# Optimization experiments

Hardware: AMD Instinct MI355X
Metric: run time of the kernel (lower is better)

## Reference

```python
import jax, jax.numpy as jnp
import numpy as np
from jax import lax


def _dtw_normalized(x, y):
    """DTW with symmetric2 step pattern and cityblock (L1) local cost on scalars.

    D[0,0] = d[0,0]; D[i,0] = D[i-1,0] + d[i,0]; D[0,j] = D[0,j-1] + d[0,j]
    D[i,j] = min(D[i-1,j-1] + 2*d, D[i-1,j] + d, D[i,j-1] + d)
    normalizedDistance = D[n-1,m-1] / (n + m)
    """
    n = x.shape[0]

    def row_update(d_prev, xi):
        d = jnp.abs(xi - y)              # local cost row, [m]
        first = d_prev[0] + d[0]         # D[i,0]

        def step(left, inp):
            dj, up, diag = inp
            val = jnp.minimum(jnp.minimum(diag + 2.0 * dj, up + dj), left + dj)
            return val, val

        _, rest = lax.scan(step, first, (d[1:], d_prev[1:], d_prev[:-1]))
        new_row = jnp.concatenate([first[None], rest])
        return new_row, None

    d0 = jnp.cumsum(jnp.abs(x[0] - y))   # D[0, :]
    d_last, _ = lax.scan(row_update, d0, x[1:])
    return d_last[-1] / (2.0 * n)        # n + m with n == m


def setup_inputs() -> dict:
    key = jax.random.key(0)
    k1, k2 = jax.random.split(key)
    x = jax.random.normal(k1, (64, 1024), dtype=jnp.float32)
    x_target = jax.random.normal(k2, (64, 1024), dtype=jnp.float32)
    return {"x": x, "x_target": x_target}


def reference(x, x_target):
    dists = jax.vmap(_dtw_normalized)(x, x_target)  # [bs]
    return jnp.mean(dists)
```

## Files before the change

kernel.cpp:

```cpp
#include <hip/hip_runtime.h>

#define SEQ_N 1024
#define BATCH 64
#define NW    4
#define RPL   4
#define KSL   32
#define DELTA 96
#define LAG   33
#define RINGN 160
#define PAD_F 352
#define PAD_B 384

__device__ __forceinline__ float wave_shr1(float v, float fill) {
    return __int_as_float(__builtin_amdgcn_update_dpp(
        __float_as_int(fill), __float_as_int(v), 0x138, 0xF, 0xF, false));
}

__global__ __launch_bounds__(256, 1) void dtw_kernel(const float* __restrict__ x,
                                                     const float* __restrict__ y,
                                                     float* __restrict__ dists) {
    __shared__ float sy_raw[PAD_F + SEQ_N + PAD_B];
    __shared__ float ring[NW - 1][RINGN];

    const int b   = blockIdx.x;
    const int tid = threadIdx.x;
    const int w   = tid >> 6;
    const int l   = tid & 63;
    const float INF = 3.0e37f;
    const int  off = w * DELTA + l;
    const bool is_ring_l0 = (l == 0) && (w > 0);
    const bool is_tid0 = (tid == 0);

    for (int i = tid; i < PAD_F; i += 256) sy_raw[i] = 0.0f;
    for (int i = tid; i < PAD_B; i += 256) sy_raw[PAD_F + SEQ_N + i] = 0.0f;
    ((float4*)(sy_raw + PAD_F))[tid] = ((const float4*)(y + b * SEQ_N))[tid];
    const float4 xv = *((const float4*)(x + b * SEQ_N + w * 256 + l * RPL));
    const float xr0 = xv.x, xr1 = xv.y, xr2 = xv.z, xr3 = xv.w;
    __syncthreads();

    const float* const yp = sy_raw + PAD_F - off;

    float c0 = INF, c1 = INF, c2 = INF, c3 = INF;
    float diag_top = INF, bottom = INF;
    float yA[KSL], yB[KSL], rb[KSL], bt[KSL];

    #pragma unroll
    for (int k = 0; k < KSL; ++k) yA[k] = yp[k];

#define EPOCH(MASKED, FIRST, S0, YU, YF)                                     \
  {                                                                          \
    __syncthreads();                                                         \
    if (w > 0) {                                                             \
      int rbase = ((S0) & 127) + 95; if (rbase >= 128) rbase -= 128;         \
      const float* rp = ring[w - 1] + rbase;                                 \
      _Pragma("unroll")                                                      \
      for (int k2 = 0; k2 < KSL; ++k2) rb[k2] = rp[k2];                      \
    } else {                                                                 \
      _Pragma("unroll")                                                      \
      for (int k2 = 0; k2 < KSL; ++k2) rb[k2] = INF;                         \
    }                                                                        \
    _Pragma("unroll")                                                        \
    for (int k2 = 0; k2 < KSL; ++k2) YF[k2] = yp[(S0) + KSL + k2];           \
    _Pragma("unroll")                                                        \
    for (int k2 = 0; k2 < KSL; ++k2) {                                       \
      const float up_dpp = wave_shr1(bottom, INF);                           \
      float upv = is_ring_l0 ? rb[k2] : up_dpp;                              \
      if ((FIRST) && k2 == 0 && is_tid0) upv = 0.0f;      \
      const float yj = YU[k2];                                               \
      bool act = true;                                                       \
      if (MASKED) act = ((unsigned)((S0) + k2 - off) < (unsigned)SEQ_N);     \
      if (act) {                                                             \
        const float d0 = xr0 - yj, d1 = xr1 - yj,                            \
                    d2 = xr2 - yj, d3 = xr3 - yj;                            \
        const float t0 = diag_top + fabsf(d0);                               \
        const float t1 = c0 + fabsf(d1);                                     \
        const float t2 = c1 + fabsf(d2);                                     \
        const float t3 = c2 + fabsf(d3);                                     \
        float v = upv;                                                       \
        v = fminf(fminf(t0, c0), v) + fabsf(d0); c0 = v;                     \
        v = fminf(fminf(t1, c1), v) + fabsf(d1); c1 = v;                     \
        v = fminf(fminf(t2, c2), v) + fabsf(d2); c2 = v;                     \
        v = fminf(fminf(t3, c3), v) + fabsf(d3); c3 = v;                     \
        diag_top = upv; bottom = v;                                          \
      }                                                                      \
      if ((FIRST) && k2 == 0 && is_tid0) diag_top = INF; \
      bt[k2] = bottom;                                                       \
    }                                                                        \
    if (w < NW - 1 && l == 63) {                                             \
      const int mm = (S0) & 127;                                             \
      float* wp = ring[w] + mm;                                              \
      _Pragma("unroll")                                                      \
      for (int k2 = 0; k2 < KSL; ++k2) wp[k2] = bt[k2];                      \
      if (mm == 0) {                                                         \
        _Pragma("unroll")                                                    \
        for (int k2 = 0; k2 < KSL; ++k2) ring[w][128 + k2] = bt[k2];         \
      }                                                                      \
    }                                                                        \
  }

    EPOCH(true, true, 0, yA, yB);
    int s0 = 32;
    for (int it = 0; it < 5; ++it) {
        EPOCH(true, false, s0, yB, yA);
        EPOCH(true, false, s0 + 32, yA, yB);
        s0 += 64;
    }
    for (int it = 0; it < 10; ++it) {
        EPOCH(false, false, s0, yB, yA);
        EPOCH(false, false, s0 + 32, yA, yB);
        s0 += 64;
    }
    for (int it = 0; it < 6; ++it) {
        EPOCH(true, false, s0, yB, yA);
        EPOCH(true, false, s0 + 32, yA, yB);
        s0 += 64;
    }
#undef EPOCH

    if (tid == 255) dists[b] = c3 * (1.0f / (2.0f * (float)SEQ_N));
}

__global__ void dtw_reduce_kernel(const float* __restrict__ dists,
                                  float* __restrict__ out) {
    float v = dists[threadIdx.x] * (1.0f / (float)BATCH);
    #pragma unroll
    for (int o = 32; o > 0; o >>= 1) v += __shfl_down(v, o);
    if (threadIdx.x == 0) out[0] = v;
}

extern "C" void kernel_launch(void* const* d_in, const int* in_sizes, int n_in,
                              void* d_out, int out_size, void* d_ws, size_t ws_size,
                              hipStream_t stream) {
    const float* x = (const float*)d_in[0];
    const float* y = (const float*)d_in[1];
    float* out = (float*)d_out;
    float* dists = (float*)d_ws;

    dtw_kernel<<<BATCH, 256, 0, stream>>>(x, y, dists);
    dtw_reduce_kernel<<<1, BATCH, 0, stream>>>(dists, out);
}
```

Baseline: 89.02 us.

## Split DTW into bidirectional half-sweeps meeting at middle column and stitch

Each batch's DTW is split into a forward sweep over the first 512 columns and a backward sweep over the reversed last 512 columns, run as separate blocks (128 blocks instead of 64). A new stitch kernel combines the two half-cost columns at the midpoint by taking a minimum over rows. This halves the serial wavefront length per block and uses more CUs. In exchange the backward sweep carries extra local-cost state, there is an extra kernel launch and workspace traffic, and the stitch logic at the boundary must be exact for correctness.

```diff
diff --git a/kernel.cpp b/kernel.cpp
--- a/kernel.cpp
+++ b/kernel.cpp
@@ -3,56 +3,74 @@
 #define SEQ_N 1024
 #define BATCH 64
 #define NW    4
-#define RPL   4
 #define KSL   32
 #define DELTA 96
-#define LAG   33
 #define RINGN 160
 #define PAD_F 352
 #define PAD_B 384
+#define NPAIR 512
+#define SYN   (PAD_F + NPAIR + PAD_B)
 
 __device__ __forceinline__ float wave_shr1(float v, float fill) {
     return __int_as_float(__builtin_amdgcn_update_dpp(
         __float_as_int(fill), __float_as_int(v), 0x138, 0xF, 0xF, false));
 }
 
-__global__ __launch_bounds__(256, 1) void dtw_kernel(const float* __restrict__ x,
-                                                     const float* __restrict__ y,
-                                                     float* __restrict__ dists) {
-    __shared__ float sy_raw[PAD_F + SEQ_N + PAD_B];
-    __shared__ float ring[NW - 1][RINGN];
-
-    const int b   = blockIdx.x;
+__global__ __launch_bounds__(256, 1) void dtw_sweep_kernel(const float* __restrict__ x,
+                                                           const float* __restrict__ y,
+                                                           float* __restrict__ wsF,
+                                                           float* __restrict__ wsP) {
+    __shared__ float  sy_raw[SYN];
+    __shared__ float  ringF[NW - 1][RINGN];
+    __shared__ float2 ringB[NW - 1][RINGN];
+
+    const int bid = blockIdx.x;
+    const int dir = bid >> 6;
+    const int b   = bid & 63;
     const int tid = threadIdx.x;
     const int w   = tid >> 6;
     const int l   = tid & 63;
     const float INF = 3.0e37f;
     const int  off = w * DELTA + l;
     const bool is_ring_l0 = (l == 0) && (w > 0);
-    const bool is_tid0 = (tid == 0);
+    const bool is_seed = (tid == 0);
+    const int  r0 = w * 256 + l * 4;
 
     for (int i = tid; i < PAD_F; i += 256) sy_raw[i] = 0.0f;
-    for (int i = tid; i < PAD_B; i += 256) sy_raw[PAD_F + SEQ_N + i] = 0.0f;
-    ((float4*)(sy_raw + PAD_F))[tid] = ((const float4*)(y + b * SEQ_N))[tid];
-    const float4 xv = *((const float4*)(x + b * SEQ_N + w * 256 + l * RPL));
-    const float xr0 = xv.x, xr1 = xv.y, xr2 = xv.z, xr3 = xv.w;
+    for (int i = tid; i < PAD_B; i += 256) sy_raw[PAD_F + NPAIR + i] = 0.0f;
+    if (tid < NPAIR / 4) {
+        if (dir == 0) {
+            ((float4*)(sy_raw + PAD_F))[tid] = ((const float4*)(y + b * SEQ_N))[tid];
+        } else {
+            const float4 v = *((const float4*)(y + b * SEQ_N + 1020 - 4 * tid));
+            ((float4*)(sy_raw + PAD_F))[tid] = make_float4(v.w, v.z, v.y, v.x);
+        }
+    }
+    float xr0, xr1, xr2, xr3;
+    if (dir == 0) {
+        const float4 v = *((const float4*)(x + b * SEQ_N + r0));
+        xr0 = v.x; xr1 = v.y; xr2 = v.z; xr3 = v.w;
+    } else {
+        const float4 v = *((const float4*)(x + b * SEQ_N + 1020 - r0));
+        xr0 = v.w; xr1 = v.z; xr2 = v.y; xr3 = v.x;
+    }
     __syncthreads();
 
     const float* const yp = sy_raw + PAD_F - off;
 
-    float c0 = INF, c1 = INF, c2 = INF, c3 = INF;
-    float diag_top = INF, bottom = INF;
-    float yA[KSL], yB[KSL], rb[KSL], bt[KSL];
-
-    #pragma unroll
-    for (int k = 0; k < KSL; ++k) yA[k] = yp[k];
-
-#define EPOCH(MASKED, FIRST, S0, YU, YF)                                     \
+    if (dir == 0) {
+        float c0 = INF, c1 = INF, c2 = INF, c3 = INF;
+        float diag_top = INF, bottom = INF;
+        float yA[KSL], yB[KSL], rb[KSL], bt[KSL];
+        #pragma unroll
+        for (int k = 0; k < KSL; ++k) yA[k] = yp[k];
+
+#define FEPOCH(MASKED, FIRST, S0, YU, YF)                                    \
   {                                                                          \
     __syncthreads();                                                         \
     if (w > 0) {                                                             \
       int rbase = ((S0) & 127) + 95; if (rbase >= 128) rbase -= 128;         \
-      const float* rp = ring[w - 1] + rbase;                                 \
+      const float* rp = ringF[w - 1] + rbase;                                \
       _Pragma("unroll")                                                      \
       for (int k2 = 0; k2 < KSL; ++k2) rb[k2] = rp[k2];                      \
     } else {                                                                 \
@@ -65,10 +83,10 @@
     for (int k2 = 0; k2 < KSL; ++k2) {                                       \
       const float up_dpp = wave_shr1(bottom, INF);                           \
       float upv = is_ring_l0 ? rb[k2] : up_dpp;                              \
-      if ((FIRST) && k2 == 0 && is_tid0) upv = 0.0f;      \
+      if ((FIRST) && k2 == 0 && is_seed) upv = 0.0f;                         \
       const float yj = YU[k2];                                               \
       bool act = true;                                                       \
-      if (MASKED) act = ((unsigned)((S0) + k2 - off) < (unsigned)SEQ_N);     \
+      if (MASKED) act = ((unsigned)((S0) + k2 - off) < (unsigned)NPAIR);     \
       if (act) {                                                             \
         const float d0 = xr0 - yj, d1 = xr1 - yj,                            \
                     d2 = xr2 - yj, d3 = xr3 - yj;                            \
@@ -83,41 +101,159 @@
         v = fminf(fminf(t3, c3), v) + fabsf(d3); c3 = v;                     \
         diag_top = upv; bottom = v;                                          \
       }                                                                      \
-      if ((FIRST) && k2 == 0 && is_tid0) diag_top = INF; \
+      if ((FIRST) && k2 == 0 && is_seed) diag_top = INF;                     \
       bt[k2] = bottom;                                                       \
     }                                                                        \
     if (w < NW - 1 && l == 63) {                                             \
       const int mm = (S0) & 127;                                             \
-      float* wp = ring[w] + mm;                                              \
+      float* wp = ringF[w] + mm;                                             \
       _Pragma("unroll")                                                      \
       for (int k2 = 0; k2 < KSL; ++k2) wp[k2] = bt[k2];                      \
       if (mm == 0) {                                                         \
         _Pragma("unroll")                                                    \
-        for (int k2 = 0; k2 < KSL; ++k2) ring[w][128 + k2] = bt[k2];         \
+        for (int k2 = 0; k2 < KSL; ++k2) ringF[w][128 + k2] = bt[k2];        \
       }                                                                      \
     }                                                                        \
   }
-
-    EPOCH(true, true, 0, yA, yB);
-    int s0 = 32;
-    for (int it = 0; it < 5; ++it) {
-        EPOCH(true, false, s0, yB, yA);
-        EPOCH(true, false, s0 + 32, yA, yB);
-        s0 += 64;
-    }
-    for (int it = 0; it < 10; ++it) {
-        EPOCH(false, false, s0, yB, yA);
-        EPOCH(false, false, s0 + 32, yA, yB);
-        s0 += 64;
-    }
-    for (int it = 0; it < 6; ++it) {
-        EPOCH(true, false, s0, yB, yA);
-        EPOCH(true, false, s0 + 32, yA, yB);
-        s0 += 64;
-    }
-#undef EPOCH
-
-    if (tid == 255) dists[b] = c3 * (1.0f / (2.0f * (float)SEQ_N));
+        FEPOCH(true, true, 0, yA, yB);
+        int s0 = 32;
+        for (int it = 0; it < 5; ++it) {
+            FEPOCH(true, false, s0, yB, yA);
+            FEPOCH(true, false, s0 + 32, yA, yB);
+            s0 += 64;
+        }
+        for (int it = 0; it < 2; ++it) {
+            FEPOCH(false, false, s0, yB, yA);
+            FEPOCH(false, false, s0 + 32, yA, yB);
+            s0 += 64;
+        }
+        FEPOCH(false, false, s0, yB, yA); s0 += 32;
+        for (int it = 0; it < 5; ++it) {
+            FEPOCH(true, false, s0, yA, yB);
+            FEPOCH(true, false, s0 + 32, yB, yA);
+            s0 += 64;
+        }
+        FEPOCH(true, false, s0, yA, yB);
+#undef FEPOCH
+        *((float4*)(wsF + b * SEQ_N + r0)) = make_float4(c0, c1, c2, c3);
+    } else {
+        float cP0 = INF, cP1 = INF, cP2 = INF, cP3 = INF;
+        float cD0 = 0.f, cD1 = 0.f, cD2 = 0.f, cD3 = 0.f;
+        float diag_P = INF, diag_D = 0.f;
+        float botP = INF, botD = 0.f;
+        float yA[KSL], yB[KSL];
+        float2 rb2[KSL], bt2[KSL];
+        #pragma unroll
+        for (int k = 0; k < KSL; ++k) yA[k] = yp[k];
+
+#define BEPOCH(MASKED, FIRST, S0, YU, YF)                                    \
+  {                                                                          \
+    __syncthreads();                                                         \
+    if (w > 0) {                                                             \
+      int rbase = ((S0) & 127) + 95; if (rbase >= 128) rbase -= 128;         \
+      const float2* rp = ringB[w - 1] + rbase;                               \
+      _Pragma("unroll")                                                      \
+      for (int k2 = 0; k2 < KSL; ++k2) rb2[k2] = rp[k2];                     \
+    } else {                                                                 \
+      _Pragma("unroll")                                                      \
+      for (int k2 = 0; k2 < KSL; ++k2) rb2[k2] = make_float2(INF, 0.f);      \
+    }                                                                        \
+    _Pragma("unroll")                                                        \
+    for (int k2 = 0; k2 < KSL; ++k2) YF[k2] = yp[(S0) + KSL + k2];           \
+    _Pragma("unroll")                                                        \
+    for (int k2 = 0; k2 < KSL; ++k2) {                                       \
+      float upP = wave_shr1(botP, INF);                                      \
+      float upD = wave_shr1(botD, 0.0f);                                     \
+      if (is_ring_l0) { upP = rb2[k2].x; upD = rb2[k2].y; }                  \
+      if ((FIRST) && k2 == 0 && is_seed) upP = 0.0f;        \
+      const float yj = YU[k2];                                               \
+      bool act = true;                                                       \
+      if (MASKED) act = ((unsigned)((S0) + k2 - off) < (unsigned)NPAIR);     \
+      if (act) {                                                             \
+        const float f0 = xr0 - yj, f1 = xr1 - yj,                            \
+                    f2 = xr2 - yj, f3 = xr3 - yj;                            \
+        const float t0 = diag_P + fabsf(diag_D);                             \
+        const float t1 = cP0 + fabsf(cD0);                                   \
+        const float t2 = cP1 + fabsf(cD1);                                   \
+        const float t3 = cP2 + fabsf(cD2);                                   \
+        float Bv = fminf(fminf(t0, upP), cP0);                               \
+        const float P0 = Bv + fabsf(f0);                                     \
+        Bv = fminf(fminf(t1, P0), cP1); const float P1 = Bv + fabsf(f1);     \
+        Bv = fminf(fminf(t2, P1), cP2); const float P2 = Bv + fabsf(f2);     \
+        Bv = fminf(fminf(t3, P2), cP3); const float P3 = Bv + fabsf(f3);     \
+        cP0 = P0; cP1 = P1; cP2 = P2; cP3 = P3;                              \
+        cD0 = f0; cD1 = f1; cD2 = f2; cD3 = f3;                              \
+        diag_P = upP; diag_D = upD;                                          \
+        botP = P3; botD = f3;                                                \
+      }                                                                      \
+      if ((FIRST) && k2 == 0 && is_seed) diag_P = INF;   \
+      bt2[k2] = make_float2(botP, botD);                                     \
+    }                                                                        \
+    if (w < NW - 1 && l == 63) {                                             \
+      const int mm = (S0) & 127;                                             \
+      float2* wp = ringB[w] + mm;                                            \
+      _Pragma("unroll")                                                      \
+      for (int k2 = 0; k2 < KSL; ++k2) wp[k2] = bt2[k2];                     \
+      if (mm == 0) {                                                         \
+        _Pragma("unroll")                                                    \
+        for (int k2 = 0; k2 < KSL; ++k2) ringB[w][128 + k2] = bt2[k2];       \
+      }                                                                      \
+    }                                                                        \
+  }
+        BEPOCH(true, true, 0, yA, yB);
+        int s0 = 32;
+        for (int it = 0; it < 5; ++it) {
+            BEPOCH(true, false, s0, yB, yA);
+            BEPOCH(true, false, s0 + 32, yA, yB);
+            s0 += 64;
+        }
+        for (int it = 0; it < 2; ++it) {
+            BEPOCH(false, false, s0, yB, yA);
+            BEPOCH(false, false, s0 + 32, yA, yB);
+            s0 += 64;
+        }
+        BEPOCH(false, false, s0, yB, yA); s0 += 32;
+        for (int it = 0; it < 5; ++it) {
+            BEPOCH(true, false, s0, yA, yB);
+            BEPOCH(true, false, s0 + 32, yB, yA);
+            s0 += 64;
+        }
+        BEPOCH(true, false, s0, yA, yB);
+#undef BEPOCH
+        *((float4*)(wsP + b * SEQ_N + 1020 - r0)) = make_float4(cP3, cP2, cP1, cP0);
+    }
+}
+
+__global__ void dtw_stitch_kernel(const float* __restrict__ x,
+                                  const float* __restrict__ y,
+                                  const float* __restrict__ wsF,
+                                  const float* __restrict__ wsP,
+                                  float* __restrict__ dists) {
+    __shared__ float red[4];
+    const int b = blockIdx.x, t = threadIdx.x;
+    const float INF = 3.0e37f;
+    const float y512 = y[b * SEQ_N + 512];
+    const float4 Fv = ((const float4*)(wsF + b * SEQ_N))[t];
+    const float4 Pv = ((const float4*)(wsP + b * SEQ_N))[t];
+    const float Pn4 = (t < 255) ? wsP[b * SEQ_N + 4 * t + 4] : INF;
+    const float F[4]  = {Fv.x, Fv.y, Fv.z, Fv.w};
+    const float P[4]  = {Pv.x, Pv.y, Pv.z, Pv.w};
+    const float Pn[4] = {Pv.y, Pv.z, Pv.w, Pn4};
+    float m = INF;
+    #pragma unroll
+    for (int k = 0; k < 4; ++k) {
+        const int i = 4 * t + k;
+        const float xn = (i < 1023) ? x[b * SEQ_N + i + 1] : 0.f;
+        const float alt = (i < 1023) ? Pn[k] + fabsf(xn - y512) : INF;
+        m = fminf(m, F[k] + fminf(P[k], alt));
+    }
+    #pragma unroll
+    for (int o = 32; o > 0; o >>= 1) m = fminf(m, __shfl_down(m, o));
+    if ((t & 63) == 0) red[t >> 6] = m;
+    __syncthreads();
+    if (t == 0)
+        dists[b] = fminf(fminf(red[0], red[1]), fminf(red[2], red[3]))
+                   * (1.0f / (2.0f * (float)SEQ_N));
 }
 
 __global__ void dtw_reduce_kernel(const float* __restrict__ dists,
@@ -134,8 +270,11 @@
     const float* x = (const float*)d_in[0];
     const float* y = (const float*)d_in[1];
     float* out = (float*)d_out;
-    float* dists = (float*)d_ws;
-
-    dtw_kernel<<<BATCH, 256, 0, stream>>>(x, y, dists);
+    float* wsF   = (float*)d_ws;
+    float* wsP   = wsF + BATCH * SEQ_N;
+    float* dists = wsP + BATCH * SEQ_N;
+
+    dtw_sweep_kernel<<<2 * BATCH, 256, 0, stream>>>(x, y, wsF, wsP);
+    dtw_stitch_kernel<<<BATCH, 256, 0, stream>>>(x, y, wsF, wsP, dists);
     dtw_reduce_kernel<<<1, BATCH, 0, stream>>>(dists, out);
 }
```

After: 85.98 us. 3.4% less time.
